# Performance work log

Hardware: AMD Instinct MI355X
Metric: run time of the kernel (lower is better)

Reference implementation:

```python
import jax, jax.numpy as jnp
import numpy as np

B, V, E, D_IN, D_OUT = 8, 10000, 160000, 128, 128
BN_EPS = 1e-5


def setup_inputs() -> dict:
    key = jax.random.key(0)
    ks = jax.random.split(key, 8)
    X = jax.random.normal(ks[0], (B, V, D_IN), dtype=jnp.float32)
    edge_attr = jax.random.normal(ks[1], (B, E), dtype=jnp.float32)
    W_node = jax.random.normal(ks[2], (D_OUT, D_IN), dtype=jnp.float32) * (1.0 / np.sqrt(D_IN))
    W_edge = jax.random.normal(ks[3], (D_OUT, 1), dtype=jnp.float32)
    W_self = jax.random.normal(ks[4], (D_OUT, D_IN), dtype=jnp.float32) * (1.0 / np.sqrt(D_IN))
    b_self = jax.random.normal(ks[5], (D_OUT,), dtype=jnp.float32) * 0.01
    gamma = jnp.ones((D_OUT,), dtype=jnp.float32)
    beta = jnp.zeros((D_OUT,), dtype=jnp.float32)
    edge_index = jax.random.randint(ks[6], (E, 2), 0, V, dtype=jnp.int32)
    return {"X": X, "edge_attr": edge_attr, "W_node": W_node, "W_edge": W_edge,
            "W_self": W_self, "b_self": b_self, "gamma": gamma, "beta": beta,
            "edge_index": edge_index}


def reference(X, edge_attr, W_node, W_edge, W_self, b_self, gamma, beta, edge_index):
    src = edge_index[:, 0]  # [E]
    dst = edge_index[:, 1]  # [E]
    # self-loop linear
    H = jnp.einsum('bvf,of->bvo', X, W_self) + b_self  # [B,V,D_OUT]
    # fused gather -> per-edge message -> scatter-add
    msg = jnp.einsum('bef,of->beo', X[:, src, :], W_node)  # [B,E,D_OUT]
    msg = msg + edge_attr[:, :, None] * W_edge[:, 0][None, None, :]
    aggregated = jnp.zeros_like(H).at[:, dst, :].add(msg)
    H = H + aggregated
    # BatchNorm1d over channel dim (training mode, biased variance over B*V)
    mean = jnp.mean(H, axis=(0, 1))
    var = jnp.var(H, axis=(0, 1))
    Hn = (H - mean) * jax.lax.rsqrt(var + BN_EPS) * gamma + beta
    return jax.nn.relu(Hn)
```

## Files before the change

kernel.cpp:

```cpp
#include <hip/hip_runtime.h>
#include <hip/hip_cooperative_groups.h>

namespace cg = cooperative_groups;

#define B_ 8
#define V_ 10000
#define E_ 160000
#define DIN 128
#define DOUT 128
#define M_ (B_*V_)
#define NINV (1.0f/80000.0f)
#define BN_EPS 1e-5f

#define GEMM_BLOCKS 625

#define WS_COUNTS  0
#define WS_SUM     10000
#define WS_SUMSQ   10128
#define WS_ROWPTR  10512
#define WS_CURSOR  20513
#define WS_SSRC    30513
#define WS_EAS     190520
#define WS_S       1470520
#define WS_WPK     1550520
#define WS_XH      1566904
#define WS_AH      6686904
#define WS_PART    11806904
#define WS_ZERO_UNITS 10000

typedef __attribute__((ext_vector_type(2))) _Float16 half2_t;
typedef __attribute__((ext_vector_type(4))) _Float16 half4_t;
typedef __attribute__((ext_vector_type(8))) _Float16 half8_t;
typedef __attribute__((ext_vector_type(4))) float f32x4;

__device__ inline half2_t i2h(unsigned i) {
    half2_t h; __builtin_memcpy(&h, &i, 4); return h;
}
__device__ inline unsigned h2i(half2_t h) {
    unsigned i; __builtin_memcpy(&i, &h, 4); return i;
}

__global__ __launch_bounds__(256) void prep_kernel(
    const float* __restrict__ X, _Float16* __restrict__ Xh,
    const float* __restrict__ Wself, const float* __restrict__ Wnode,
    _Float16* __restrict__ Wpk,
    const int* __restrict__ EI, int* __restrict__ counts)
{
    const int blk = blockIdx.x;
    const int t = threadIdx.x;
    if (blk < 10000) {
        int idx = blk * 256 + t;
        float4 v = ((const float4*)X)[idx];
        half4_t o = { (_Float16)v.x, (_Float16)v.y, (_Float16)v.z, (_Float16)v.w };
        ((half4_t*)Xh)[idx] = o;
    } else if (blk < 10016) {
        int g = (blk - 10000) * 256 + t;
        int pair = g >> 6;
        int lane = g & 63;
        int ks = pair >> 3;
        int nt = pair & 7;
        int o = nt * 16 + (lane & 15);
        int k = ks * 32 + (lane >> 4) * 8;
        const float* wsrc = (k < 128) ? (Wself + o * 128 + k)
                                      : (Wnode + o * 128 + (k - 128));
        _Float16* dst = Wpk + ((size_t)pair * 64 + lane) * 8;
#pragma unroll
        for (int j = 0; j < 8; ++j) dst[j] = (_Float16)wsrc[j];
    } else {
        int e = (blk - 10016) * 256 + t;
        if (e < E_) atomicAdd(&counts[EI[2 * e + 1]], 1);
    }
}

__global__ __launch_bounds__(256) void scan_kernel(
    const int* __restrict__ counts, int* __restrict__ row_ptr,
    int* __restrict__ cursor)
{
    __shared__ int psum[256];
    const int t = threadIdx.x;
    const int base = t * 40;
    int local[40];
    int s = 0;
#pragma unroll
    for (int i = 0; i < 40; ++i) {
        int idx = base + i;
        int c = (idx < V_) ? counts[idx] : 0;
        local[i] = s;
        s += c;
    }
    psum[t] = s;
    __syncthreads();
    for (int off = 1; off < 256; off <<= 1) {
        int v = (t >= off) ? psum[t - off] : 0;
        __syncthreads();
        psum[t] += v;
        __syncthreads();
    }
    int excl = (t == 0) ? 0 : psum[t - 1];
#pragma unroll
    for (int i = 0; i < 40; ++i) {
        int idx = base + i;
        if (idx < V_) {
            int rp = excl + local[i];
            row_ptr[idx] = rp;
            cursor[idx] = rp;
        }
    }
    if (t == 255) row_ptr[V_] = psum[255];
}

__global__ __launch_bounds__(256) void bucket_kernel(
    const int* __restrict__ EI, const float* __restrict__ EA,
    int* __restrict__ cursor, int* __restrict__ ssrc,
    float* __restrict__ EAs)
{
    int e = blockIdx.x * 256 + threadIdx.x;
    if (e < E_) {
        int src = EI[2 * e];
        int dst = EI[2 * e + 1];
        int p = atomicAdd(&cursor[dst], 1);
        ssrc[p] = src;
        float4 v0, v1;
        v0.x = EA[0 * E_ + e]; v0.y = EA[1 * E_ + e];
        v0.z = EA[2 * E_ + e]; v0.w = EA[3 * E_ + e];
        v1.x = EA[4 * E_ + e]; v1.y = EA[5 * E_ + e];
        v1.z = EA[6 * E_ + e]; v1.w = EA[7 * E_ + e];
        *(float4*)(EAs + (size_t)p * 8) = v0;
        *(float4*)(EAs + (size_t)p * 8 + 4) = v1;
    }
}

__global__ __launch_bounds__(256) void gather_kernel(
    const _Float16* __restrict__ Xh, const float* __restrict__ EAs,
    const int* __restrict__ row_ptr, const int* __restrict__ ssrc,
    _Float16* __restrict__ Ah, float* __restrict__ S)
{
    const int b = blockIdx.x & 7;
    const int dblk = blockIdx.x >> 3;
    const int w = threadIdx.x >> 6;
    const int lane = threadIdx.x & 63;
    const int q = lane >> 4;
    const int sl = lane & 15;
    const int d = dblk * 4 + w;
    const int wid = b * V_ + d;
    const int k0 = row_ptr[d];
    const int k1 = row_ptr[d + 1];
    const _Float16* Xb = Xh + (size_t)b * V_ * DIN + sl * 8;
    half2_t a0 = (half2_t)0, a1 = (half2_t)0, a2 = (half2_t)0, a3 = (half2_t)0;
    float ea = 0.0f;
    for (int kb = k0; kb < k1; kb += 64) {
        int cnt = min(64, k1 - kb);
        int msrc = 0;
        if (lane < cnt) {
            msrc = ssrc[kb + lane];
            ea += EAs[(size_t)(kb + lane) * 8 + b];
        }
        int j = 0;
        for (; j + 16 <= cnt; j += 16) {
#pragma unroll
            for (int u = 0; u < 4; ++u) {
                int s = __shfl(msrc, j + u * 4 + q);
                uint4 v = *(const uint4*)(Xb + (size_t)s * DIN);
                a0 += i2h(v.x); a1 += i2h(v.y); a2 += i2h(v.z); a3 += i2h(v.w);
            }
        }
        for (; j + 4 <= cnt; j += 4) {
            int s = __shfl(msrc, j + q);
            uint4 v = *(const uint4*)(Xb + (size_t)s * DIN);
            a0 += i2h(v.x); a1 += i2h(v.y); a2 += i2h(v.z); a3 += i2h(v.w);
        }
        if (j < cnt) {
            int s = __shfl(msrc, j + q);
            if (j + q < cnt) {
                uint4 v = *(const uint4*)(Xb + (size_t)s * DIN);
                a0 += i2h(v.x); a1 += i2h(v.y); a2 += i2h(v.z); a3 += i2h(v.w);
            }
        }
    }
#pragma unroll
    for (int off = 32; off >= 16; off >>= 1) {
        a0 += i2h(__shfl_down(h2i(a0), off));
        a1 += i2h(__shfl_down(h2i(a1), off));
        a2 += i2h(__shfl_down(h2i(a2), off));
        a3 += i2h(__shfl_down(h2i(a3), off));
    }
    for (int off = 32; off; off >>= 1) ea += __shfl_down(ea, off);
    if (lane == 0) S[wid] = ea;
    if (lane < 16) {
        uint4 o;
        o.x = h2i(a0); o.y = h2i(a1); o.z = h2i(a2); o.w = h2i(a3);
        *(uint4*)(Ah + (size_t)wid * DIN + sl * 8) = o;
    }
}

__device__ __forceinline__ void gemm_body(
    const _Float16* __restrict__ Xh, const _Float16* __restrict__ Ah,
    const _Float16* __restrict__ Wpk, const float* __restrict__ S,
    const float* __restrict__ bself, const float* __restrict__ wedge,
    int bid, int t, f32x4 (&acc)[2][8], float* cs, float* css)
{
    const int wave = t >> 6;
    const int lane = t & 63;
    const int quad = lane >> 4;
    const int ln = lane & 15;
    const int rowbase = bid * 128 + wave * 32;
    const int m0 = rowbase + ln;
    const int m1 = rowbase + 16 + ln;

    if (t < 128) { cs[t] = 0.0f; css[t] = 0.0f; }

#pragma unroll
    for (int mt = 0; mt < 2; ++mt)
#pragma unroll
        for (int nt = 0; nt < 8; ++nt) acc[mt][nt] = (f32x4){0.f, 0.f, 0.f, 0.f};

    const _Float16* X0 = Xh + (size_t)m0 * DIN + quad * 8;
    const _Float16* X1 = Xh + (size_t)m1 * DIN + quad * 8;
    const _Float16* A0 = Ah + (size_t)m0 * DIN + quad * 8;
    const _Float16* A1 = Ah + (size_t)m1 * DIN + quad * 8;
    const _Float16* Wl = Wpk + lane * 8;

#pragma unroll
    for (int ks = 0; ks < 8; ++ks) {
        half8_t af0, af1;
        if (ks < 4) {
            af0 = *(const half8_t*)(X0 + ks * 32);
            af1 = *(const half8_t*)(X1 + ks * 32);
        } else {
            af0 = *(const half8_t*)(A0 + (ks - 4) * 32);
            af1 = *(const half8_t*)(A1 + (ks - 4) * 32);
        }
#pragma unroll
        for (int nt = 0; nt < 8; ++nt) {
            half8_t bfr = *(const half8_t*)(Wl + (size_t)(ks * 8 + nt) * 512);
            acc[0][nt] = __builtin_amdgcn_mfma_f32_16x16x32_f16(af0, bfr, acc[0][nt], 0, 0, 0);
            acc[1][nt] = __builtin_amdgcn_mfma_f32_16x16x32_f16(af1, bfr, acc[1][nt], 0, 0, 0);
        }
    }

    float bs[8], we[8];
#pragma unroll
    for (int nt = 0; nt < 8; ++nt) {
        int c = nt * 16 + ln;
        bs[nt] = bself[c];
        we[nt] = wedge[c];
    }
    float psum[8], psq[8];
#pragma unroll
    for (int nt = 0; nt < 8; ++nt) { psum[nt] = 0.0f; psq[nt] = 0.0f; }

#pragma unroll
    for (int mt = 0; mt < 2; ++mt) {
        const int rbase = rowbase + mt * 16 + quad * 4;
        float sv[4];
#pragma unroll
        for (int r = 0; r < 4; ++r) sv[r] = S[rbase + r];
#pragma unroll
        for (int nt = 0; nt < 8; ++nt) {
#pragma unroll
            for (int r = 0; r < 4; ++r) {
                float h = acc[mt][nt][r] + bs[nt] + sv[r] * we[nt];
                acc[mt][nt][r] = h;
                psum[nt] += h;
                psq[nt] += h * h;
            }
        }
    }
#pragma unroll
    for (int nt = 0; nt < 8; ++nt) {
        psum[nt] += __shfl_down(psum[nt], 32);
        psum[nt] += __shfl_down(psum[nt], 16);
        psq[nt] += __shfl_down(psq[nt], 32);
        psq[nt] += __shfl_down(psq[nt], 16);
    }
    __syncthreads();
    if (lane < 16) {
#pragma unroll
        for (int nt = 0; nt < 8; ++nt) {
            atomicAdd(&cs[nt * 16 + ln], psum[nt]);
            atomicAdd(&css[nt * 16 + ln], psq[nt]);
        }
    }
    __syncthreads();
}

__global__ __launch_bounds__(256, 4) void gemm_norm_coop_kernel(
    const _Float16* __restrict__ Xh, const _Float16* __restrict__ Ah,
    const _Float16* __restrict__ Wpk, const float* __restrict__ S,
    const float* __restrict__ bself, const float* __restrict__ wedge,
    const float* __restrict__ gamma, const float* __restrict__ beta,
    float* __restrict__ H, float* __restrict__ Partials,
    float* __restrict__ gsum, float* __restrict__ gsumsq)
{
    __shared__ float cs[128];
    __shared__ float css[128];
    const int t = threadIdx.x;
    f32x4 acc[2][8];
    gemm_body(Xh, Ah, Wpk, S, bself, wedge, blockIdx.x, t, acc, cs, css);

    Partials[(size_t)blockIdx.x * 256 + t] = (t < 128) ? cs[t] : css[t - 128];
    __threadfence();
    cg::this_grid().sync();

    if (blockIdx.x < 256 && t < 64) {
        const int c = blockIdx.x;
        float a = 0.0f;
        for (int p = t; p < GEMM_BLOCKS; p += 64)
            a += Partials[(size_t)p * 256 + c];
        for (int off = 32; off; off >>= 1) a += __shfl_down(a, off);
        if (t == 0) {
            if (c < 128) gsum[c] = a;
            else gsumsq[c - 128] = a;
        }
        __threadfence();
    }
    cg::this_grid().sync();

    const int wave = t >> 6;
    const int lane = t & 63;
    const int quad = lane >> 4;
    const int ln = lane & 15;
    const int rowbase = blockIdx.x * 128 + wave * 32;
    float scl[8], shf[8];
#pragma unroll
    for (int nt = 0; nt < 8; ++nt) {
        int c = nt * 16 + ln;
        float gs = __hip_atomic_load(&gsum[c], __ATOMIC_RELAXED,
                                     __HIP_MEMORY_SCOPE_AGENT);
        float gq = __hip_atomic_load(&gsumsq[c], __ATOMIC_RELAXED,
                                     __HIP_MEMORY_SCOPE_AGENT);
        float mean = gs * NINV;
        float rstd = rsqrtf(gq * NINV - mean * mean + BN_EPS);
        scl[nt] = gamma[c] * rstd;
        shf[nt] = beta[c] - mean * scl[nt];
    }
#pragma unroll
    for (int mt = 0; mt < 2; ++mt) {
        const int rbase = rowbase + mt * 16 + quad * 4;
#pragma unroll
        for (int r = 0; r < 4; ++r) {
            float* Hr = H + (size_t)(rbase + r) * DOUT + ln;
#pragma unroll
            for (int nt = 0; nt < 8; ++nt)
                Hr[nt * 16] = fmaxf(acc[mt][nt][r] * scl[nt] + shf[nt], 0.0f);
        }
    }
}

__global__ __launch_bounds__(256) void mfma_gemm_kernel(
    const _Float16* __restrict__ Xh, const _Float16* __restrict__ Ah,
    const _Float16* __restrict__ Wpk, const float* __restrict__ S,
    const float* __restrict__ bself, const float* __restrict__ wedge,
    float* __restrict__ H, float* __restrict__ Partials)
{
    __shared__ float cs[128];
    __shared__ float css[128];
    const int t = threadIdx.x;
    f32x4 acc[2][8];
    gemm_body(Xh, Ah, Wpk, S, bself, wedge, blockIdx.x, t, acc, cs, css);

    const int wave = t >> 6;
    const int lane = t & 63;
    const int quad = lane >> 4;
    const int ln = lane & 15;
    const int rowbase = blockIdx.x * 128 + wave * 32;
#pragma unroll
    for (int mt = 0; mt < 2; ++mt) {
        const int rbase = rowbase + mt * 16 + quad * 4;
#pragma unroll
        for (int r = 0; r < 4; ++r) {
            float* Hr = H + (size_t)(rbase + r) * DOUT + ln;
#pragma unroll
            for (int nt = 0; nt < 8; ++nt)
                Hr[nt * 16] = acc[mt][nt][r];
        }
    }
    Partials[(size_t)blockIdx.x * 256 + t] = (t < 128) ? cs[t] : css[t - 128];
}

__global__ __launch_bounds__(64) void reduce_stats_kernel(
    const float* __restrict__ Partials, float* __restrict__ gsum,
    float* __restrict__ gsumsq)
{
    const int c = blockIdx.x;
    const int t = threadIdx.x;
    float acc = 0.0f;
    for (int p = t; p < GEMM_BLOCKS; p += 64)
        acc += Partials[(size_t)p * 256 + c];
    for (int off = 32; off; off >>= 1) acc += __shfl_down(acc, off);
    if (t == 0) {
        if (c < 128) gsum[c] = acc;
        else gsumsq[c - 128] = acc;
    }
}

__global__ __launch_bounds__(256) void norm_relu_kernel(
    float* __restrict__ H, const float* __restrict__ gsum,
    const float* __restrict__ gsumsq, const float* __restrict__ gamma,
    const float* __restrict__ beta)
{
    int idx = blockIdx.x * 256 + threadIdx.x;
    int o4 = (idx & 31) * 4;
    float4 s = *(const float4*)(gsum + o4);
    float4 q = *(const float4*)(gsumsq + o4);
    float4 g = *(const float4*)(gamma + o4);
    float4 bt = *(const float4*)(beta + o4);
    float4 sc, sh;
    {
        float m0 = s.x * NINV, m1 = s.y * NINV, m2 = s.z * NINV, m3 = s.w * NINV;
        float r0 = rsqrtf(q.x * NINV - m0 * m0 + BN_EPS);
        float r1 = rsqrtf(q.y * NINV - m1 * m1 + BN_EPS);
        float r2 = rsqrtf(q.z * NINV - m2 * m2 + BN_EPS);
        float r3 = rsqrtf(q.w * NINV - m3 * m3 + BN_EPS);
        sc.x = g.x * r0; sc.y = g.y * r1; sc.z = g.z * r2; sc.w = g.w * r3;
        sh.x = bt.x - m0 * sc.x; sh.y = bt.y - m1 * sc.y;
        sh.z = bt.z - m2 * sc.z; sh.w = bt.w - m3 * sc.w;
    }
    float4 h = ((const float4*)H)[idx];
    h.x = fmaxf(h.x * sc.x + sh.x, 0.0f);
    h.y = fmaxf(h.y * sc.y + sh.y, 0.0f);
    h.z = fmaxf(h.z * sc.z + sh.z, 0.0f);
    h.w = fmaxf(h.w * sc.w + sh.w, 0.0f);
    ((float4*)H)[idx] = h;
}

extern "C" void kernel_launch(void* const* d_in, const int* in_sizes, int n_in,
                              void* d_out, int out_size, void* d_ws, size_t ws_size,
                              hipStream_t stream)
{
    const float* X      = (const float*)d_in[0];
    const float* EA     = (const float*)d_in[1];
    const float* Wnode  = (const float*)d_in[2];
    const float* Wedge  = (const float*)d_in[3];
    const float* Wself  = (const float*)d_in[4];
    const float* bself  = (const float*)d_in[5];
    const float* gamma  = (const float*)d_in[6];
    const float* beta   = (const float*)d_in[7];
    const int*   EI     = (const int*)d_in[8];

    int*   wsI    = (int*)d_ws;
    float* wsF    = (float*)d_ws;
    int*   counts = wsI + WS_COUNTS;
    float* gsum   = wsF + WS_SUM;
    float* gsumsq = wsF + WS_SUMSQ;
    int*   rowptr = wsI + WS_ROWPTR;
    int*   cursor = wsI + WS_CURSOR;
    int*   ssrc   = wsI + WS_SSRC;
    float* EAs    = wsF + WS_EAS;
    float* S      = wsF + WS_S;
    _Float16* Wpk = (_Float16*)(wsI + WS_WPK);
    _Float16* Xh  = (_Float16*)(wsI + WS_XH);
    _Float16* Ah  = (_Float16*)(wsI + WS_AH);
    float* Partials = wsF + WS_PART;
    float* H      = (float*)d_out;

    hipMemsetAsync(d_ws, 0, (size_t)WS_ZERO_UNITS * 4, stream);

    prep_kernel<<<10641, 256, 0, stream>>>(X, Xh, Wself, Wnode, Wpk, EI, counts);
    scan_kernel<<<1, 256, 0, stream>>>(counts, rowptr, cursor);
    bucket_kernel<<<(E_ + 255) / 256, 256, 0, stream>>>(EI, EA, cursor, ssrc, EAs);

    gather_kernel<<<M_ / 4, 256, 0, stream>>>(Xh, EAs, rowptr, ssrc, Ah, S);

    int blocksPerCU = 0;
    hipError_t qerr = hipOccupancyMaxActiveBlocksPerMultiprocessor(
        &blocksPerCU, gemm_norm_coop_kernel, 256, 0);
    bool coop = (qerr == hipSuccess) && (blocksPerCU * 256 >= GEMM_BLOCKS);
    if (coop) {
        void* args[] = { (void*)&Xh, (void*)&Ah, (void*)&Wpk, (void*)&S,
                         (void*)&bself, (void*)&Wedge, (void*)&gamma,
                         (void*)&beta, (void*)&H, (void*)&Partials,
                         (void*)&gsum, (void*)&gsumsq };
        hipError_t lerr = hipLaunchCooperativeKernel(
            (void*)gemm_norm_coop_kernel, dim3(GEMM_BLOCKS), dim3(256),
            args, 0, stream);
        if (lerr == hipSuccess) return;
    }
    mfma_gemm_kernel<<<GEMM_BLOCKS, 256, 0, stream>>>(Xh, Ah, Wpk, S, bself,
                                                      Wedge, H, Partials);
    reduce_stats_kernel<<<256, 64, 0, stream>>>(Partials, gsum, gsumsq);
    norm_relu_kernel<<<(M_ * DOUT / 4) / 256, 256, 0, stream>>>(H, gsum, gsumsq,
                                                                gamma, beta);
}
```

Before: 221.8 us.

## Replace cooperative grid-sync GEMM with two-pass recompute GEMM for batchnorm stats

Removes the cooperative launch and its two grid-wide syncs. A first GEMM pass computes only the per-channel sum and sum-of-squares partials, a small kernel folds them into scale and shift, and a second GEMM pass recomputes the outputs and applies normalization and ReLU before a single store. This trades redundant MFMA work and a second read of the fp16 activations for avoiding grid barriers and an extra read-modify-write of H.

```diff
diff --git a/kernel.cpp b/kernel.cpp
--- a/kernel.cpp
+++ b/kernel.cpp
@@ -1,7 +1,4 @@
 #include <hip/hip_runtime.h>
-#include <hip/hip_cooperative_groups.h>
-
-namespace cg = cooperative_groups;
 
 #define B_ 8
 #define V_ 10000
@@ -15,8 +12,8 @@
 #define GEMM_BLOCKS 625
 
 #define WS_COUNTS  0
-#define WS_SUM     10000
-#define WS_SUMSQ   10128
+#define WS_SCL     10000
+#define WS_SHF     10128
 #define WS_ROWPTR  10512
 #define WS_CURSOR  20513
 #define WS_SSRC    30513
@@ -193,6 +190,7 @@
     }
 }
 
+template<bool STATS>
 __device__ __forceinline__ void gemm_body(
     const _Float16* __restrict__ Xh, const _Float16* __restrict__ Ah,
     const _Float16* __restrict__ Wpk, const float* __restrict__ S,
@@ -207,7 +205,9 @@
     const int m0 = rowbase + ln;
     const int m1 = rowbase + 16 + ln;
 
-    if (t < 128) { cs[t] = 0.0f; css[t] = 0.0f; }
+    if constexpr (STATS) {
+        if (t < 128) { cs[t] = 0.0f; css[t] = 0.0f; }
+    }
 
 #pragma unroll
     for (int mt = 0; mt < 2; ++mt)
@@ -246,8 +246,10 @@
         we[nt] = wedge[c];
     }
     float psum[8], psq[8];
-#pragma unroll
-    for (int nt = 0; nt < 8; ++nt) { psum[nt] = 0.0f; psq[nt] = 0.0f; }
+    if constexpr (STATS) {
+#pragma unroll
+        for (int nt = 0; nt < 8; ++nt) { psum[nt] = 0.0f; psq[nt] = 0.0f; }
+    }
 
 #pragma unroll
     for (int mt = 0; mt < 2; ++mt) {
@@ -261,78 +263,95 @@
             for (int r = 0; r < 4; ++r) {
                 float h = acc[mt][nt][r] + bs[nt] + sv[r] * we[nt];
                 acc[mt][nt][r] = h;
-                psum[nt] += h;
-                psq[nt] += h * h;
+                if constexpr (STATS) {
+                    psum[nt] += h;
+                    psq[nt] += h * h;
+                }
             }
         }
     }
-#pragma unroll
-    for (int nt = 0; nt < 8; ++nt) {
-        psum[nt] += __shfl_down(psum[nt], 32);
-        psum[nt] += __shfl_down(psum[nt], 16);
-        psq[nt] += __shfl_down(psq[nt], 32);
-        psq[nt] += __shfl_down(psq[nt], 16);
-    }
-    __syncthreads();
-    if (lane < 16) {
+    if constexpr (STATS) {
 #pragma unroll
         for (int nt = 0; nt < 8; ++nt) {
-            atomicAdd(&cs[nt * 16 + ln], psum[nt]);
-            atomicAdd(&css[nt * 16 + ln], psq[nt]);
-        }
-    }
-    __syncthreads();
-}
-
-__global__ __launch_bounds__(256, 4) void gemm_norm_coop_kernel(
+            psum[nt] += __shfl_down(psum[nt], 32);
+            psum[nt] += __shfl_down(psum[nt], 16);
+            psq[nt] += __shfl_down(psq[nt], 32);
+            psq[nt] += __shfl_down(psq[nt], 16);
+        }
+        __syncthreads();
+        if (lane < 16) {
+#pragma unroll
+            for (int nt = 0; nt < 8; ++nt) {
+                atomicAdd(&cs[nt * 16 + ln], psum[nt]);
+                atomicAdd(&css[nt * 16 + ln], psq[nt]);
+            }
+        }
+        __syncthreads();
+    }
+}
+
+__global__ __launch_bounds__(256) void stats_gemm_kernel(
     const _Float16* __restrict__ Xh, const _Float16* __restrict__ Ah,
     const _Float16* __restrict__ Wpk, const float* __restrict__ S,
     const float* __restrict__ bself, const float* __restrict__ wedge,
-    const float* __restrict__ gamma, const float* __restrict__ beta,
-    float* __restrict__ H, float* __restrict__ Partials,
-    float* __restrict__ gsum, float* __restrict__ gsumsq)
+    float* __restrict__ Partials)
 {
     __shared__ float cs[128];
     __shared__ float css[128];
     const int t = threadIdx.x;
     f32x4 acc[2][8];
-    gemm_body(Xh, Ah, Wpk, S, bself, wedge, blockIdx.x, t, acc, cs, css);
-
+    gemm_body<true>(Xh, Ah, Wpk, S, bself, wedge, blockIdx.x, t, acc, cs, css);
     Partials[(size_t)blockIdx.x * 256 + t] = (t < 128) ? cs[t] : css[t - 128];
-    __threadfence();
-    cg::this_grid().sync();
-
-    if (blockIdx.x < 256 && t < 64) {
-        const int c = blockIdx.x;
-        float a = 0.0f;
-        for (int p = t; p < GEMM_BLOCKS; p += 64)
-            a += Partials[(size_t)p * 256 + c];
-        for (int off = 32; off; off >>= 1) a += __shfl_down(a, off);
-        if (t == 0) {
-            if (c < 128) gsum[c] = a;
-            else gsumsq[c - 128] = a;
-        }
-        __threadfence();
-    }
-    cg::this_grid().sync();
+}
+
+__global__ __launch_bounds__(64) void finalize_stats_kernel(
+    const float* __restrict__ Partials, const float* __restrict__ gamma,
+    const float* __restrict__ beta, float* __restrict__ scl,
+    float* __restrict__ shf)
+{
+    const int c = blockIdx.x;
+    const int t = threadIdx.x;
+    float s = 0.0f, q = 0.0f;
+    for (int p = t; p < GEMM_BLOCKS; p += 64) {
+        s += Partials[(size_t)p * 256 + c];
+        q += Partials[(size_t)p * 256 + 128 + c];
+    }
+    for (int off = 32; off; off >>= 1) {
+        s += __shfl_down(s, off);
+        q += __shfl_down(q, off);
+    }
+    if (t == 0) {
+        float mean = s * NINV;
+        float rstd = rsqrtf(q * NINV - mean * mean + BN_EPS);
+        float sc = gamma[c] * rstd;
+        scl[c] = sc;
+        shf[c] = beta[c] - mean * sc;
+    }
+}
+
+__global__ __launch_bounds__(256) void norm_gemm_kernel(
+    const _Float16* __restrict__ Xh, const _Float16* __restrict__ Ah,
+    const _Float16* __restrict__ Wpk, const float* __restrict__ S,
+    const float* __restrict__ bself, const float* __restrict__ wedge,
+    const float* __restrict__ scl, const float* __restrict__ shf,
+    float* __restrict__ H)
+{
+    const int t = threadIdx.x;
+    f32x4 acc[2][8];
+    gemm_body<false>(Xh, Ah, Wpk, S, bself, wedge, blockIdx.x, t, acc,
+                     nullptr, nullptr);
 
     const int wave = t >> 6;
     const int lane = t & 63;
     const int quad = lane >> 4;
     const int ln = lane & 15;
     const int rowbase = blockIdx.x * 128 + wave * 32;
-    float scl[8], shf[8];
+    float sc[8], sh[8];
 #pragma unroll
     for (int nt = 0; nt < 8; ++nt) {
         int c = nt * 16 + ln;
-        float gs = __hip_atomic_load(&gsum[c], __ATOMIC_RELAXED,
-                                     __HIP_MEMORY_SCOPE_AGENT);
-        float gq = __hip_atomic_load(&gsumsq[c], __ATOMIC_RELAXED,
-                                     __HIP_MEMORY_SCOPE_AGENT);
-        float mean = gs * NINV;
-        float rstd = rsqrtf(gq * NINV - mean * mean + BN_EPS);
-        scl[nt] = gamma[c] * rstd;
-        shf[nt] = beta[c] - mean * scl[nt];
+        sc[nt] = scl[c];
+        sh[nt] = shf[c];
     }
 #pragma unroll
     for (int mt = 0; mt < 2; ++mt) {
@@ -342,86 +361,9 @@
             float* Hr = H + (size_t)(rbase + r) * DOUT + ln;
 #pragma unroll
             for (int nt = 0; nt < 8; ++nt)
-                Hr[nt * 16] = fmaxf(acc[mt][nt][r] * scl[nt] + shf[nt], 0.0f);
-        }
-    }
-}
-
-__global__ __launch_bounds__(256) void mfma_gemm_kernel(
-    const _Float16* __restrict__ Xh, const _Float16* __restrict__ Ah,
-    const _Float16* __restrict__ Wpk, const float* __restrict__ S,
-    const float* __restrict__ bself, const float* __restrict__ wedge,
-    float* __restrict__ H, float* __restrict__ Partials)
-{
-    __shared__ float cs[128];
-    __shared__ float css[128];
-    const int t = threadIdx.x;
-    f32x4 acc[2][8];
-    gemm_body(Xh, Ah, Wpk, S, bself, wedge, blockIdx.x, t, acc, cs, css);
-
-    const int wave = t >> 6;
-    const int lane = t & 63;
-    const int quad = lane >> 4;
-    const int ln = lane & 15;
-    const int rowbase = blockIdx.x * 128 + wave * 32;
-#pragma unroll
-    for (int mt = 0; mt < 2; ++mt) {
-        const int rbase = rowbase + mt * 16 + quad * 4;
-#pragma unroll
-        for (int r = 0; r < 4; ++r) {
-            float* Hr = H + (size_t)(rbase + r) * DOUT + ln;
-#pragma unroll
-            for (int nt = 0; nt < 8; ++nt)
-                Hr[nt * 16] = acc[mt][nt][r];
-        }
-    }
-    Partials[(size_t)blockIdx.x * 256 + t] = (t < 128) ? cs[t] : css[t - 128];
-}
-
-__global__ __launch_bounds__(64) void reduce_stats_kernel(
-    const float* __restrict__ Partials, float* __restrict__ gsum,
-    float* __restrict__ gsumsq)
-{
-    const int c = blockIdx.x;
-    const int t = threadIdx.x;
-    float acc = 0.0f;
-    for (int p = t; p < GEMM_BLOCKS; p += 64)
-        acc += Partials[(size_t)p * 256 + c];
-    for (int off = 32; off; off >>= 1) acc += __shfl_down(acc, off);
-    if (t == 0) {
-        if (c < 128) gsum[c] = acc;
-        else gsumsq[c - 128] = acc;
-    }
-}
-
-__global__ __launch_bounds__(256) void norm_relu_kernel(
-    float* __restrict__ H, const float* __restrict__ gsum,
-    const float* __restrict__ gsumsq, const float* __restrict__ gamma,
-    const float* __restrict__ beta)
-{
-    int idx = blockIdx.x * 256 + threadIdx.x;
-    int o4 = (idx & 31) * 4;
-    float4 s = *(const float4*)(gsum + o4);
-    float4 q = *(const float4*)(gsumsq + o4);
-    float4 g = *(const float4*)(gamma + o4);
-    float4 bt = *(const float4*)(beta + o4);
-    float4 sc, sh;
-    {
-        float m0 = s.x * NINV, m1 = s.y * NINV, m2 = s.z * NINV, m3 = s.w * NINV;
-        float r0 = rsqrtf(q.x * NINV - m0 * m0 + BN_EPS);
-        float r1 = rsqrtf(q.y * NINV - m1 * m1 + BN_EPS);
-        float r2 = rsqrtf(q.z * NINV - m2 * m2 + BN_EPS);
-        float r3 = rsqrtf(q.w * NINV - m3 * m3 + BN_EPS);
-        sc.x = g.x * r0; sc.y = g.y * r1; sc.z = g.z * r2; sc.w = g.w * r3;
-        sh.x = bt.x - m0 * sc.x; sh.y = bt.y - m1 * sc.y;
-        sh.z = bt.z - m2 * sc.z; sh.w = bt.w - m3 * sc.w;
-    }
-    float4 h = ((const float4*)H)[idx];
-    h.x = fmaxf(h.x * sc.x + sh.x, 0.0f);
-    h.y = fmaxf(h.y * sc.y + sh.y, 0.0f);
-    h.z = fmaxf(h.z * sc.z + sh.z, 0.0f);
-    h.w = fmaxf(h.w * sc.w + sh.w, 0.0f);
-    ((float4*)H)[idx] = h;
+                Hr[nt * 16] = fmaxf(acc[mt][nt][r] * sc[nt] + sh[nt], 0.0f);
+        }
+    }
 }
 
 extern "C" void kernel_launch(void* const* d_in, const int* in_sizes, int n_in,
@@ -441,8 +383,8 @@
     int*   wsI    = (int*)d_ws;
     float* wsF    = (float*)d_ws;
     int*   counts = wsI + WS_COUNTS;
-    float* gsum   = wsF + WS_SUM;
-    float* gsumsq = wsF + WS_SUMSQ;
+    float* scl    = wsF + WS_SCL;
+    float* shf    = wsF + WS_SHF;
     int*   rowptr = wsI + WS_ROWPTR;
     int*   cursor = wsI + WS_CURSOR;
     int*   ssrc   = wsI + WS_SSRC;
@@ -462,23 +404,9 @@
 
     gather_kernel<<<M_ / 4, 256, 0, stream>>>(Xh, EAs, rowptr, ssrc, Ah, S);
 
-    int blocksPerCU = 0;
-    hipError_t qerr = hipOccupancyMaxActiveBlocksPerMultiprocessor(
-        &blocksPerCU, gemm_norm_coop_kernel, 256, 0);
-    bool coop = (qerr == hipSuccess) && (blocksPerCU * 256 >= GEMM_BLOCKS);
-    if (coop) {
-        void* args[] = { (void*)&Xh, (void*)&Ah, (void*)&Wpk, (void*)&S,
-                         (void*)&bself, (void*)&Wedge, (void*)&gamma,
-                         (void*)&beta, (void*)&H, (void*)&Partials,
-                         (void*)&gsum, (void*)&gsumsq };
-        hipError_t lerr = hipLaunchCooperativeKernel(
-            (void*)gemm_norm_coop_kernel, dim3(GEMM_BLOCKS), dim3(256),
-            args, 0, stream);
-        if (lerr == hipSuccess) return;
-    }
-    mfma_gemm_kernel<<<GEMM_BLOCKS, 256, 0, stream>>>(Xh, Ah, Wpk, S, bself,
-                                                      Wedge, H, Partials);
-    reduce_stats_kernel<<<256, 64, 0, stream>>>(Partials, gsum, gsumsq);
-    norm_relu_kernel<<<(M_ * DOUT / 4) / 256, 256, 0, stream>>>(H, gsum, gsumsq,
-                                                                gamma, beta);
-}
+    stats_gemm_kernel<<<GEMM_BLOCKS, 256, 0, stream>>>(Xh, Ah, Wpk, S, bself,
+                                                       Wedge, Partials);
+    finalize_stats_kernel<<<128, 64, 0, stream>>>(Partials, gamma, beta, scl, shf);
+    norm_gemm_kernel<<<GEMM_BLOCKS, 256, 0, stream>>>(Xh, Ah, Wpk, S, bself,
+                                                      Wedge, scl, shf, H);
+}
```

Measured after the change: 234.7 us. 1.06x slower.
